# Kernel tuning notes

Hardware: AMD Instinct MI355X
Metric: run time of the kernel (lower is better)

The kernel has to match this reference:

```python
import jax, jax.numpy as jnp
import numpy as np

N, C, F_CAT, F_NUM, V = 250000, 32, 16, 16, 64


def setup_inputs() -> dict:
    key = jax.random.key(0)
    k0, k1, k2, k3, k4, k5 = jax.random.split(key, 6)
    X_cat = jax.random.randint(k0, (N, F_CAT), 0, V)
    X_num = jax.random.normal(k1, (N, F_NUM), dtype=jnp.float32)
    class_probs = jax.random.uniform(k2, (C,), dtype=jnp.float32)
    class_probs = class_probs / class_probs.sum()
    # conditional probs are smoothed counts/size_class in fit(); keep them positive
    cat_probs = jax.random.uniform(k3, (C, F_CAT, V), dtype=jnp.float32) * 0.9 + 0.05
    means = jax.random.normal(k4, (C, F_NUM), dtype=jnp.float32)
    stds = jax.random.uniform(k5, (C, F_NUM), dtype=jnp.float32) + 0.5  # keep away from 0
    return {"X_cat": X_cat, "X_num": X_num, "class_probs": class_probs,
            "cat_probs": cat_probs, "means": means, "stds": stds}


def reference(X_cat, X_num, class_probs, cat_probs, means, stds):
    # X_cat: [N, F_cat] int indices; X_num: [N, F_num] float
    # cat_probs: [C, F_cat, V]; means/stds: [C, F_num]; class_probs: [C]
    C_, Fc, _ = cat_probs.shape
    # categorical gather -> [N, C, F_cat]
    ci = jnp.arange(C_)[None, :, None]
    fi = jnp.arange(Fc)[None, None, :]
    gathered = cat_probs[ci, fi, X_cat[:, None, :]]
    cat_term = jnp.prod(gathered, axis=-1)            # [N, C]
    # gaussian likelihood (faithful to module: 1/(2*pi*std^2) * exp(-0.5*z^2))
    pi = jnp.float32(np.pi)
    x = X_num[:, None, :]                             # [N, 1, F_num]
    z = (x - means[None]) / stds[None]
    lik = 1.0 / (2.0 * pi * stds[None] ** 2) * jnp.exp(-0.5 * z ** 2)  # [N, C, F_num]
    num_term = jnp.prod(lik, axis=-1)                 # [N, C]
    pred_probs = class_probs[None, :] * cat_term * num_term
    return jnp.argmax(pred_probs, axis=1)
```

## Files before the change

kernel.cpp:

```cpp
#include <hip/hip_runtime.h>
#include <math.h>

constexpr int kN  = 250000;
constexpr int kC  = 32;
constexpr int kFC = 16;
constexpr int kFN = 16;
constexpr int kV  = 64;
constexpr int kBlock = 1024;

constexpr int kRowDw = 36;

constexpr int    kTabOffDw    = 1088;
constexpr size_t kWsNeedBytes = (size_t)(kTabOffDw + 1024 * kC) * 4;


__global__ __launch_bounds__(256) void nbc_prep(
    const float* __restrict__ class_probs,
    const float* __restrict__ means,
    const float* __restrict__ stds,
    const float* __restrict__ cat_probs,
    float* __restrict__ ws,
    int use_tab)
{
    const int b = blockIdx.x;
    const int t = threadIdx.x;
    if (b == 0) {
        const float two_pi = 2.0f * (float)M_PI;
        for (int i = t; i < kC * kFN; i += 256) {
            float m  = means[i];
            float s  = stds[i];
            float rs = 1.0f / s;
            ws[2 * i]     = -0.5f * rs * rs;
            ws[2 * i + 1] = m * rs * rs;
        }
        if (t < kC) {
            float k = logf(class_probs[t]);
            for (int f = 0; f < kFN; ++f) {
                float s  = stds[t * kFN + f];
                float m  = means[t * kFN + f];
                float rs = 1.0f / s;
                k += logf(1.0f / (two_pi * (s * s)));
                k += -0.5f * (m * rs) * (m * rs);
            }
            ws[1024 + t] = k;
        }
    } else if (use_tab) {
        const int base = (b - 1) * 1024;
        for (int k2 = 0; k2 < 4; ++k2) {
            int s = base + t + k2 * 256;
            int c = s >> 10;
            int r = s & 1023;
            ws[kTabOffDw + r * 32 + c] = logf(cat_probs[s]);
        }
    }
}

__global__ __launch_bounds__(kBlock) void nbc_main(
    const int*   __restrict__ X_cat,
    const float* __restrict__ X_num,
    const float* __restrict__ class_probs,
    const float* __restrict__ cat_probs,
    const float* __restrict__ means,
    const float* __restrict__ stds,
    const float* __restrict__ ws,
    int* __restrict__ out,
    int use_tab)
{
    __shared__ float lcat[1024 * kRowDw];

    const int tid = threadIdx.x;
    const int n   = blockIdx.x * kBlock + tid;
    const bool active = (n < kN);

    unsigned pack[4];
    float    x[kFN];
    if (active) {
        const int4* p4 = reinterpret_cast<const int4*>(X_cat + (size_t)n * kFC);
        int4 a0 = p4[0], a1 = p4[1], a2 = p4[2], a3 = p4[3];
        pack[0] = (unsigned)a0.x | ((unsigned)a0.y << 8) |
                  ((unsigned)a0.z << 16) | ((unsigned)a0.w << 24);
        pack[1] = (unsigned)a1.x | ((unsigned)a1.y << 8) |
                  ((unsigned)a1.z << 16) | ((unsigned)a1.w << 24);
        pack[2] = (unsigned)a2.x | ((unsigned)a2.y << 8) |
                  ((unsigned)a2.z << 16) | ((unsigned)a2.w << 24);
        pack[3] = (unsigned)a3.x | ((unsigned)a3.y << 8) |
                  ((unsigned)a3.z << 16) | ((unsigned)a3.w << 24);

        const float4* q4 = reinterpret_cast<const float4*>(X_num + (size_t)n * kFN);
        float4 b0 = q4[0], b1 = q4[1], b2 = q4[2], b3 = q4[3];
        x[0]=b0.x;  x[1]=b0.y;  x[2]=b0.z;  x[3]=b0.w;
        x[4]=b1.x;  x[5]=b1.y;  x[6]=b1.z;  x[7]=b1.w;
        x[8]=b2.x;  x[9]=b2.y;  x[10]=b2.z; x[11]=b2.w;
        x[12]=b3.x; x[13]=b3.y; x[14]=b3.z; x[15]=b3.w;
    } else {
        pack[0] = pack[1] = pack[2] = pack[3] = 0u;
        #pragma unroll
        for (int f = 0; f < kFN; ++f) x[f] = 0.0f;
    }

    if (use_tab) {
        const float4* __restrict__ lt4 =
            reinterpret_cast<const float4*>(ws + kTabOffDw);
        #pragma unroll
        for (int i = 0; i < 8; ++i) {
            int j = i * kBlock + tid;
            float4 w = lt4[j];
            int r  = j >> 3;
            int cg = j & 7;
            *reinterpret_cast<float4*>(lcat + r * kRowDw + cg * 4) = w;
        }
    } else {
        #pragma unroll
        for (int cg = 0; cg < 8; ++cg) {
            float4 w;
            w.x = logf(cat_probs[(size_t)(cg * 4 + 0) * 1024 + tid]);
            w.y = logf(cat_probs[(size_t)(cg * 4 + 1) * 1024 + tid]);
            w.z = logf(cat_probs[(size_t)(cg * 4 + 2) * 1024 + tid]);
            w.w = logf(cat_probs[(size_t)(cg * 4 + 3) * 1024 + tid]);
            *reinterpret_cast<float4*>(lcat + (size_t)tid * kRowDw + cg * 4) = w;
        }
    }
    __syncthreads();

    if (!active) return;

    int rowdw[kFC];
    #pragma unroll
    for (int f = 0; f < kFC; ++f) {
        const int v = (pack[f >> 2] >> ((f & 3) * 8)) & 63;
        rowdw[f] = ((f << 6) + v) * kRowDw;
    }

    const float2* __restrict__ P = reinterpret_cast<const float2*>(ws);
    const float*  __restrict__ K = ws + 1024;

    float best = -INFINITY, second = -INFINITY;
    int   besti = 0;

    #pragma unroll 1
    for (int grp = 0; grp < 8; ++grp) {
        const int cbase = grp << 2;
        float acc[4];

        #pragma unroll
        for (int j = 0; j < 4; ++j) {
            const int c = cbase + j;
            float a = K[c];
            #pragma unroll
            for (int f = 0; f < kFN; ++f) {
                float2 p = P[(c << 4) + f];
                a = fmaf(x[f], fmaf(x[f], p.x, p.y), a);
            }
            acc[j] = a;
        }

        #pragma unroll
        for (int f = 0; f < kFC; ++f) {
            const float4 t = *reinterpret_cast<const float4*>(
                &lcat[rowdw[f] + (grp << 2)]);
            acc[0] += t.x;
            acc[1] += t.y;
            acc[2] += t.z;
            acc[3] += t.w;
        }

        #pragma unroll
        for (int j = 0; j < 4; ++j) {
            float T = acc[j];
            if (T > best)        { second = best; best = T; besti = cbase + j; }
            else if (T > second) { second = T; }
        }
    }

    if (best >= -86.0f && (best - second) >= 8.0e-3f) {
        out[n] = besti;
        return;
    }

    const float thr    = (best >= -86.0f) ? (best - 1.6e-2f) : -INFINITY;
    const float two_pi = 2.0f * (float)M_PI;
    float bb = -INFINITY;
    int   bi = 0;

    for (int c = 0; c < kC; ++c) {
        float a = K[c];
        #pragma unroll
        for (int f = 0; f < kFN; ++f) {
            float2 p = P[(c << 4) + f];
            a = fmaf(x[f], fmaf(x[f], p.x, p.y), a);
        }
        #pragma unroll
        for (int f = 0; f < kFC; ++f) {
            a += lcat[rowdw[f] + c];
        }

        if (a >= thr) {
            const float* __restrict__ row = cat_probs + (size_t)c * (kFC * kV);
            float cat = row[pack[0] & 63];
            #pragma unroll
            for (int f = 1; f < kFC; ++f) {
                const int v = (pack[f >> 2] >> ((f & 3) * 8)) & 63;
                cat *= row[(f << 6) + v];
            }
            float num;
            #pragma unroll
            for (int f = 0; f < kFN; ++f) {
                float m = means[c * kFN + f];
                float s = stds [c * kFN + f];
                float inv = 1.0f / (two_pi * (s * s));
                float z = (x[f] - m) / s;
                float e = expf(-0.5f * (z * z));
                float lik = inv * e;
                num = (f == 0) ? lik : num * lik;
            }
            float pred = (class_probs[c] * cat) * num;
            if (pred > bb) { bb = pred; bi = c; }
        }
    }
    out[n] = bi;
}

extern "C" void kernel_launch(void* const* d_in, const int* in_sizes, int n_in,
                              void* d_out, int out_size, void* d_ws, size_t ws_size,
                              hipStream_t stream) {
    const int*   X_cat       = (const int*)  d_in[0];
    const float* X_num       = (const float*)d_in[1];
    const float* class_probs = (const float*)d_in[2];
    const float* cat_probs   = (const float*)d_in[3];
    const float* means       = (const float*)d_in[4];
    const float* stds        = (const float*)d_in[5];
    int*   out = (int*)d_out;
    float* ws  = (float*)d_ws;

    const int use_tab = (ws_size >= kWsNeedBytes) ? 1 : 0;

    hipLaunchKernelGGL(nbc_prep, dim3(use_tab ? 33 : 1), dim3(256), 0, stream,
                       class_probs, means, stds, cat_probs, ws, use_tab);

    dim3 block(kBlock);
    dim3 grid((kN + kBlock - 1) / kBlock);
    hipLaunchKernelGGL(nbc_main, grid, block, 0, stream,
                       X_cat, X_num, class_probs, cat_probs, means, stds, ws,
                       out, use_tab);
}
```

Measured before the change: 138.2 us.

## Split class dimension across two blocks per chunk with a merge kernel

The main kernel now runs two blocks per 1024-row chunk, each scoring 16 of the 32 classes against a halved shared-memory log table. This cuts LDS per block and lets more blocks reside per CU. Each half writes its best, second-best and argmax to workspace, and a merge kernel combines them, running the exact-probability fallback only for near-ties. In exchange it recomputes the logs per block instead of reading a precomputed table, adds a kernel launch and workspace round-trip, and reloads inputs in both halves.

```diff
diff --git a/kernel.cpp b/kernel.cpp
--- a/kernel.cpp
+++ b/kernel.cpp
@@ -8,68 +8,52 @@
 constexpr int kV  = 64;
 constexpr int kBlock = 1024;
 
-constexpr int kRowDw = 36;
-
-constexpr int    kTabOffDw    = 1088;
-constexpr size_t kWsNeedBytes = (size_t)(kTabOffDw + 1024 * kC) * 4;
+constexpr int kRowDw = 18;
+
+constexpr int    kOffRes      = 1088;
+constexpr size_t kWsNeedSplit = (size_t)(kOffRes + 6 * kN) * 4;
 
 
 __global__ __launch_bounds__(256) void nbc_prep(
     const float* __restrict__ class_probs,
     const float* __restrict__ means,
     const float* __restrict__ stds,
-    const float* __restrict__ cat_probs,
-    float* __restrict__ ws,
-    int use_tab)
+    float* __restrict__ ws)
 {
-    const int b = blockIdx.x;
     const int t = threadIdx.x;
-    if (b == 0) {
-        const float two_pi = 2.0f * (float)M_PI;
-        for (int i = t; i < kC * kFN; i += 256) {
-            float m  = means[i];
-            float s  = stds[i];
+    const float two_pi = 2.0f * (float)M_PI;
+    for (int i = t; i < kC * kFN; i += 256) {
+        float m  = means[i];
+        float s  = stds[i];
+        float rs = 1.0f / s;
+        ws[2 * i]     = -0.5f * rs * rs;
+        ws[2 * i + 1] = m * rs * rs;
+    }
+    if (t < kC) {
+        float k = logf(class_probs[t]);
+        for (int f = 0; f < kFN; ++f) {
+            float s  = stds[t * kFN + f];
+            float m  = means[t * kFN + f];
             float rs = 1.0f / s;
-            ws[2 * i]     = -0.5f * rs * rs;
-            ws[2 * i + 1] = m * rs * rs;
-        }
-        if (t < kC) {
-            float k = logf(class_probs[t]);
-            for (int f = 0; f < kFN; ++f) {
-                float s  = stds[t * kFN + f];
-                float m  = means[t * kFN + f];
-                float rs = 1.0f / s;
-                k += logf(1.0f / (two_pi * (s * s)));
-                k += -0.5f * (m * rs) * (m * rs);
-            }
-            ws[1024 + t] = k;
-        }
-    } else if (use_tab) {
-        const int base = (b - 1) * 1024;
-        for (int k2 = 0; k2 < 4; ++k2) {
-            int s = base + t + k2 * 256;
-            int c = s >> 10;
-            int r = s & 1023;
-            ws[kTabOffDw + r * 32 + c] = logf(cat_probs[s]);
-        }
+            k += logf(1.0f / (two_pi * (s * s)));
+            k += -0.5f * (m * rs) * (m * rs);
+        }
+        ws[1024 + t] = k;
     }
 }
 
-__global__ __launch_bounds__(kBlock) void nbc_main(
+__global__ __launch_bounds__(kBlock) void nbc_half(
     const int*   __restrict__ X_cat,
     const float* __restrict__ X_num,
-    const float* __restrict__ class_probs,
     const float* __restrict__ cat_probs,
-    const float* __restrict__ means,
-    const float* __restrict__ stds,
-    const float* __restrict__ ws,
-    int* __restrict__ out,
-    int use_tab)
+    float* __restrict__ ws)
 {
     __shared__ float lcat[1024 * kRowDw];
 
-    const int tid = threadIdx.x;
-    const int n   = blockIdx.x * kBlock + tid;
+    const int chunk = blockIdx.x >> 1;
+    const int half  = blockIdx.x & 1;
+    const int tid   = threadIdx.x;
+    const int n     = chunk * kBlock + tid;
     const bool active = (n < kN);
 
     unsigned pack[4];
@@ -98,26 +82,15 @@
         for (int f = 0; f < kFN; ++f) x[f] = 0.0f;
     }
 
-    if (use_tab) {
-        const float4* __restrict__ lt4 =
-            reinterpret_cast<const float4*>(ws + kTabOffDw);
-        #pragma unroll
-        for (int i = 0; i < 8; ++i) {
-            int j = i * kBlock + tid;
-            float4 w = lt4[j];
-            int r  = j >> 3;
-            int cg = j & 7;
-            *reinterpret_cast<float4*>(lcat + r * kRowDw + cg * 4) = w;
-        }
-    } else {
-        #pragma unroll
-        for (int cg = 0; cg < 8; ++cg) {
+    {
+        #pragma unroll
+        for (int q = 0; q < 4; ++q) {
             float4 w;
-            w.x = logf(cat_probs[(size_t)(cg * 4 + 0) * 1024 + tid]);
-            w.y = logf(cat_probs[(size_t)(cg * 4 + 1) * 1024 + tid]);
-            w.z = logf(cat_probs[(size_t)(cg * 4 + 2) * 1024 + tid]);
-            w.w = logf(cat_probs[(size_t)(cg * 4 + 3) * 1024 + tid]);
-            *reinterpret_cast<float4*>(lcat + (size_t)tid * kRowDw + cg * 4) = w;
+            w.x = logf(cat_probs[(size_t)((half << 4) + q * 4 + 0) * 1024 + tid]);
+            w.y = logf(cat_probs[(size_t)((half << 4) + q * 4 + 1) * 1024 + tid]);
+            w.z = logf(cat_probs[(size_t)((half << 4) + q * 4 + 2) * 1024 + tid]);
+            w.w = logf(cat_probs[(size_t)((half << 4) + q * 4 + 3) * 1024 + tid]);
+            *reinterpret_cast<float4*>(lcat + tid * kRowDw + q * 4) = w;
         }
     }
     __syncthreads();
@@ -138,8 +111,8 @@
     int   besti = 0;
 
     #pragma unroll 1
-    for (int grp = 0; grp < 8; ++grp) {
-        const int cbase = grp << 2;
+    for (int grp = 0; grp < 4; ++grp) {
+        const int cbase = (half << 4) + (grp << 2);
         float acc[4];
 
         #pragma unroll
@@ -172,6 +145,186 @@
         }
     }
 
+    ws[kOffRes + half * kN + n]          = best;
+    ws[kOffRes + 2 * kN + half * kN + n] = second;
+    reinterpret_cast<int*>(ws)[kOffRes + 4 * kN + half * kN + n] = besti;
+}
+
+__global__ __launch_bounds__(256) void nbc_merge(
+    const int*   __restrict__ X_cat,
+    const float* __restrict__ X_num,
+    const float* __restrict__ class_probs,
+    const float* __restrict__ cat_probs,
+    const float* __restrict__ means,
+    const float* __restrict__ stds,
+    const float* __restrict__ ws,
+    int* __restrict__ out)
+{
+    const int n = blockIdx.x * 256 + threadIdx.x;
+    if (n >= kN) return;
+
+    const float b0 = ws[kOffRes + n];
+    const float b1 = ws[kOffRes + kN + n];
+    const float s0 = ws[kOffRes + 2 * kN + n];
+    const float s1 = ws[kOffRes + 3 * kN + n];
+    const int   i0 = reinterpret_cast<const int*>(ws)[kOffRes + 4 * kN + n];
+    const int   i1 = reinterpret_cast<const int*>(ws)[kOffRes + 5 * kN + n];
+
+    float wb, ws2; int wi;
+    if (b1 > b0) { wb = b1; wi = i1; ws2 = fmaxf(b0, s1); }
+    else         { wb = b0; wi = i0; ws2 = fmaxf(b1, s0); }
+
+    if (wb >= -86.0f && (wb - ws2) >= 8.0e-3f) {
+        out[n] = wi;
+        return;
+    }
+
+    unsigned pack[4];
+    float    x[kFN];
+    {
+        const int4* p4 = reinterpret_cast<const int4*>(X_cat + (size_t)n * kFC);
+        int4 a0 = p4[0], a1 = p4[1], a2 = p4[2], a3 = p4[3];
+        pack[0] = (unsigned)a0.x | ((unsigned)a0.y << 8) |
+                  ((unsigned)a0.z << 16) | ((unsigned)a0.w << 24);
+        pack[1] = (unsigned)a1.x | ((unsigned)a1.y << 8) |
+                  ((unsigned)a1.z << 16) | ((unsigned)a1.w << 24);
+        pack[2] = (unsigned)a2.x | ((unsigned)a2.y << 8) |
+                  ((unsigned)a2.z << 16) | ((unsigned)a2.w << 24);
+        pack[3] = (unsigned)a3.x | ((unsigned)a3.y << 8) |
+                  ((unsigned)a3.z << 16) | ((unsigned)a3.w << 24);
+
+        const float4* q4 = reinterpret_cast<const float4*>(X_num + (size_t)n * kFN);
+        float4 c0 = q4[0], c1 = q4[1], c2 = q4[2], c3 = q4[3];
+        x[0]=c0.x;  x[1]=c0.y;  x[2]=c0.z;  x[3]=c0.w;
+        x[4]=c1.x;  x[5]=c1.y;  x[6]=c1.z;  x[7]=c1.w;
+        x[8]=c2.x;  x[9]=c2.y;  x[10]=c2.z; x[11]=c2.w;
+        x[12]=c3.x; x[13]=c3.y; x[14]=c3.z; x[15]=c3.w;
+    }
+
+    const float two_pi = 2.0f * (float)M_PI;
+    float bb = -INFINITY;
+    int   bi = 0;
+    for (int c = 0; c < kC; ++c) {
+        const float* __restrict__ row = cat_probs + (size_t)c * (kFC * kV);
+        float cat = row[pack[0] & 63];
+        #pragma unroll
+        for (int f = 1; f < kFC; ++f) {
+            const int v = (pack[f >> 2] >> ((f & 3) * 8)) & 63;
+            cat *= row[(f << 6) + v];
+        }
+        float num;
+        #pragma unroll
+        for (int f = 0; f < kFN; ++f) {
+            float m = means[c * kFN + f];
+            float s = stds [c * kFN + f];
+            float inv = 1.0f / (two_pi * (s * s));
+            float z = (x[f] - m) / s;
+            float e = expf(-0.5f * (z * z));
+            float lik = inv * e;
+            num = (f == 0) ? lik : num * lik;
+        }
+        float pred = (class_probs[c] * cat) * num;
+        if (pred > bb) { bb = pred; bi = c; }
+    }
+    out[n] = bi;
+}
+
+__global__ __launch_bounds__(kBlock) void nbc_mono(
+    const int*   __restrict__ X_cat,
+    const float* __restrict__ X_num,
+    const float* __restrict__ class_probs,
+    const float* __restrict__ cat_probs,
+    const float* __restrict__ means,
+    const float* __restrict__ stds,
+    const float* __restrict__ ws,
+    int* __restrict__ out)
+{
+    __shared__ float lcat[1024 * 36];
+
+    const int tid = threadIdx.x;
+    const int n   = blockIdx.x * kBlock + tid;
+    const bool active = (n < kN);
+
+    unsigned pack[4];
+    float    x[kFN];
+    if (active) {
+        const int4* p4 = reinterpret_cast<const int4*>(X_cat + (size_t)n * kFC);
+        int4 a0 = p4[0], a1 = p4[1], a2 = p4[2], a3 = p4[3];
+        pack[0] = (unsigned)a0.x | ((unsigned)a0.y << 8) |
+                  ((unsigned)a0.z << 16) | ((unsigned)a0.w << 24);
+        pack[1] = (unsigned)a1.x | ((unsigned)a1.y << 8) |
+                  ((unsigned)a1.z << 16) | ((unsigned)a1.w << 24);
+        pack[2] = (unsigned)a2.x | ((unsigned)a2.y << 8) |
+                  ((unsigned)a2.z << 16) | ((unsigned)a2.w << 24);
+        pack[3] = (unsigned)a3.x | ((unsigned)a3.y << 8) |
+                  ((unsigned)a3.z << 16) | ((unsigned)a3.w << 24);
+        const float4* q4 = reinterpret_cast<const float4*>(X_num + (size_t)n * kFN);
+        float4 b0 = q4[0], b1 = q4[1], b2 = q4[2], b3 = q4[3];
+        x[0]=b0.x;  x[1]=b0.y;  x[2]=b0.z;  x[3]=b0.w;
+        x[4]=b1.x;  x[5]=b1.y;  x[6]=b1.z;  x[7]=b1.w;
+        x[8]=b2.x;  x[9]=b2.y;  x[10]=b2.z; x[11]=b2.w;
+        x[12]=b3.x; x[13]=b3.y; x[14]=b3.z; x[15]=b3.w;
+    } else {
+        pack[0] = pack[1] = pack[2] = pack[3] = 0u;
+        #pragma unroll
+        for (int f = 0; f < kFN; ++f) x[f] = 0.0f;
+    }
+
+    #pragma unroll
+    for (int cg = 0; cg < 8; ++cg) {
+        float4 w;
+        w.x = logf(cat_probs[(size_t)(cg * 4 + 0) * 1024 + tid]);
+        w.y = logf(cat_probs[(size_t)(cg * 4 + 1) * 1024 + tid]);
+        w.z = logf(cat_probs[(size_t)(cg * 4 + 2) * 1024 + tid]);
+        w.w = logf(cat_probs[(size_t)(cg * 4 + 3) * 1024 + tid]);
+        *reinterpret_cast<float4*>(lcat + (size_t)tid * 36 + cg * 4) = w;
+    }
+    __syncthreads();
+
+    if (!active) return;
+
+    int rowdw[kFC];
+    #pragma unroll
+    for (int f = 0; f < kFC; ++f) {
+        const int v = (pack[f >> 2] >> ((f & 3) * 8)) & 63;
+        rowdw[f] = ((f << 6) + v) * 36;
+    }
+
+    const float2* __restrict__ P = reinterpret_cast<const float2*>(ws);
+    const float*  __restrict__ K = ws + 1024;
+
+    float best = -INFINITY, second = -INFINITY;
+    int   besti = 0;
+
+    #pragma unroll 1
+    for (int grp = 0; grp < 8; ++grp) {
+        const int cbase = grp << 2;
+        float acc[4];
+        #pragma unroll
+        for (int j = 0; j < 4; ++j) {
+            const int c = cbase + j;
+            float a = K[c];
+            #pragma unroll
+            for (int f = 0; f < kFN; ++f) {
+                float2 p = P[(c << 4) + f];
+                a = fmaf(x[f], fmaf(x[f], p.x, p.y), a);
+            }
+            acc[j] = a;
+        }
+        #pragma unroll
+        for (int f = 0; f < kFC; ++f) {
+            const float4 t = *reinterpret_cast<const float4*>(
+                &lcat[rowdw[f] + (grp << 2)]);
+            acc[0] += t.x; acc[1] += t.y; acc[2] += t.z; acc[3] += t.w;
+        }
+        #pragma unroll
+        for (int j = 0; j < 4; ++j) {
+            float T = acc[j];
+            if (T > best)        { second = best; best = T; besti = cbase + j; }
+            else if (T > second) { second = T; }
+        }
+    }
+
     if (best >= -86.0f && (best - second) >= 8.0e-3f) {
         out[n] = besti;
         return;
@@ -181,7 +334,6 @@
     const float two_pi = 2.0f * (float)M_PI;
     float bb = -INFINITY;
     int   bi = 0;
-
     for (int c = 0; c < kC; ++c) {
         float a = K[c];
         #pragma unroll
@@ -190,9 +342,7 @@
             a = fmaf(x[f], fmaf(x[f], p.x, p.y), a);
         }
         #pragma unroll
-        for (int f = 0; f < kFC; ++f) {
-            a += lcat[rowdw[f] + c];
-        }
+        for (int f = 0; f < kFC; ++f) a += lcat[rowdw[f] + c];
 
         if (a >= thr) {
             const float* __restrict__ row = cat_probs + (size_t)c * (kFC * kV);
@@ -232,14 +382,19 @@
     int*   out = (int*)d_out;
     float* ws  = (float*)d_ws;
 
-    const int use_tab = (ws_size >= kWsNeedBytes) ? 1 : 0;
-
-    hipLaunchKernelGGL(nbc_prep, dim3(use_tab ? 33 : 1), dim3(256), 0, stream,
-                       class_probs, means, stds, cat_probs, ws, use_tab);
-
-    dim3 block(kBlock);
-    dim3 grid((kN + kBlock - 1) / kBlock);
-    hipLaunchKernelGGL(nbc_main, grid, block, 0, stream,
-                       X_cat, X_num, class_probs, cat_probs, means, stds, ws,
-                       out, use_tab);
+    hipLaunchKernelGGL(nbc_prep, dim3(1), dim3(256), 0, stream,
+                       class_probs, means, stds, ws);
+
+    const int chunks = (kN + kBlock - 1) / kBlock;
+    if (ws_size >= kWsNeedSplit) {
+        hipLaunchKernelGGL(nbc_half, dim3(chunks * 2), dim3(kBlock), 0, stream,
+                           X_cat, X_num, cat_probs, ws);
+        hipLaunchKernelGGL(nbc_merge, dim3((kN + 255) / 256), dim3(256), 0, stream,
+                           X_cat, X_num, class_probs, cat_probs, means, stds,
+                           ws, out);
+    } else {
+        hipLaunchKernelGGL(nbc_mono, dim3(chunks), dim3(kBlock), 0, stream,
+                           X_cat, X_num, class_probs, cat_probs, means, stds,
+                           ws, out);
+    }
 }
```

New measurement: 343.6 us. +148.7%, slower.
